# Kernel tuning notes

Hardware: AMD Instinct MI355X
Metric: run time of the kernel (lower is better)

Reference implementation:

```python
import jax, jax.numpy as jnp
import numpy as np

# LSS grid config (nuScenes defaults)
XB, YB, ZB = (-50.0, 50.0, 0.5), (-50.0, 50.0, 0.5), (-10.0, 10.0, 20.0)
DB = (4.0, 45.0, 1.0)
OGFH, OGFW, DOWNSAMPLE = 128, 352, 16
FH, FW = OGFH // DOWNSAMPLE, OGFW // DOWNSAMPLE  # 8, 22
DX = jnp.array([XB[2], YB[2], ZB[2]], jnp.float32)
BX = jnp.array([XB[0] + XB[2] / 2, YB[0] + YB[2] / 2, ZB[0] + ZB[2] / 2], jnp.float32)
NX = np.array([int((XB[1]-XB[0])/XB[2]), int((YB[1]-YB[0])/YB[2]), int((ZB[1]-ZB[0])/ZB[2])])  # [200,200,1]


def make_frustum():
    ds = jnp.arange(DB[0], DB[1], DB[2], dtype=jnp.float32)  # [D]
    D = ds.shape[0]
    xs = jnp.linspace(0.0, OGFW - 1.0, FW, dtype=jnp.float32)
    ys = jnp.linspace(0.0, OGFH - 1.0, FH, dtype=jnp.float32)
    xs_g = jnp.broadcast_to(xs[None, None, :], (D, FH, FW))
    ys_g = jnp.broadcast_to(ys[None, :, None], (D, FH, FW))
    ds_g = jnp.broadcast_to(ds[:, None, None], (D, FH, FW))
    return jnp.stack([xs_g, ys_g, ds_g], -1)  # [D,FH,FW,3]


def setup_inputs() -> dict:
    key = jax.random.key(0)
    ks = jax.random.split(key, 8)
    B, N, D, C = 8, 6, 41, 64
    x = jax.random.normal(ks[0], (B, N, D, FH, FW, C), jnp.float32)
    eye = jnp.eye(3, dtype=jnp.float32)
    rots = eye[None, None] + 0.01 * jax.random.normal(ks[1], (B, N, 3, 3), jnp.float32)
    trans = 0.5 * jax.random.normal(ks[2], (B, N, 3), jnp.float32)
    # realistic post-augmentation intrinsics for 352x128 images
    base_intrin = jnp.array([[250.0, 0.0, 176.0], [0.0, 250.0, 64.0], [0.0, 0.0, 1.0]], jnp.float32)
    intrins = base_intrin[None, None] + 0.1 * jax.random.normal(ks[3], (B, N, 3, 3), jnp.float32)
    post_rots = eye[None, None] + 0.001 * jax.random.normal(ks[4], (B, N, 3, 3), jnp.float32)
    post_trans = 0.1 * jax.random.normal(ks[5], (B, N, 3), jnp.float32)
    return {"x": x, "rots": rots, "trans": trans, "intrins": intrins,
            "post_rots": post_rots, "post_trans": post_trans}


def _get_geometry(frustum, rots, trans, intrins, post_rots, post_trans):
    eps = 1e-6
    eye = jnp.eye(3, dtype=post_rots.dtype)
    # undo post-augmentation
    pts = frustum[None, None] - post_trans[:, :, None, None, None, :]  # [B,N,D,H,W,3]
    inv_post = jnp.linalg.inv(post_rots + eye * eps)
    pts = jnp.einsum('bnij,bndhwj->bndhwi', inv_post, pts)
    xy, d = pts[..., :2], pts[..., 2:3]
    safe_d = jnp.where(jnp.abs(d) < eps, eps * jnp.sign(d + eps), d)
    pts = jnp.concatenate([xy * safe_d, safe_d], -1)
    combine = rots @ jnp.linalg.inv(intrins + eye * eps)  # [B,N,3,3]
    pts = jnp.einsum('bnij,bndhwj->bndhwi', combine, pts)
    return pts + trans[:, :, None, None, None, :]


def _voxel_pooling(geom, x):
    # geom: [B,N,D,H,W,3], x: [B,N,D,H,W,C]
    B, N, D, H, W, C = x.shape
    nx0, nx1, nx2 = int(NX[0]), int(NX[1]), int(NX[2])
    Nprime = B * N * D * H * W
    gn = (geom - (BX - DX / 2.0)) / DX
    gi = gn.astype(jnp.int32).reshape(Nprime, 3)  # trunc toward zero like .long()
    xf = x.reshape(Nprime, C)
    kept = ((gi[:, 0] >= 0) & (gi[:, 0] < nx0) &
            (gi[:, 1] >= 0) & (gi[:, 1] < nx1) &
            (gi[:, 2] >= 0) & (gi[:, 2] < nx2))
    xf = xf * kept[:, None].astype(xf.dtype)
    gx = jnp.clip(gi[:, 0], 0, nx0 - 1)
    gy = jnp.clip(gi[:, 1], 0, nx1 - 1)
    gz = jnp.clip(gi[:, 2], 0, nx2 - 1)
    batch_ix = jnp.repeat(jnp.arange(B, dtype=jnp.int32), Nprime // B)
    # sum-per-voxel (equivalent to sort + cumsum_trick + scatter-set)
    flat = ((batch_ix * nx2 + gz) * nx0 + gx) * nx1 + gy
    pooled = jax.ops.segment_sum(xf, flat, num_segments=B * nx2 * nx0 * nx1)
    final = pooled.reshape(B, nx2, nx0, nx1, C).transpose(0, 4, 1, 2, 3)
    return final  # [B,C,nz,nx,ny]


def reference(x, rots, trans, intrins, post_rots, post_trans):
    frustum = make_frustum()
    geom = _get_geometry(frustum, rots, trans, intrins, post_rots, post_trans)
    return _voxel_pooling(geom, x)
```

## Files before the change

### kernel.cpp

```cpp
#include <hip/hip_runtime.h>
#include <math.h>

namespace {

constexpr int B  = 8;
constexpr int N  = 6;
constexpr int D  = 41;
constexpr int FH = 8;
constexpr int FW = 22;
constexpr int C  = 64;
constexpr int NPTS = B * N * D * FH * FW;
constexpr int NX0 = 200, NX1 = 200, NX2 = 1;
constexpr int NVOX = NX0 * NX1;
constexpr int NVOX_ALL = B * NVOX;
constexpr int MAT_STRIDE = 24;
constexpr size_t SCR_ELEMS = (size_t)B * NVOX * C;
constexpr size_t SCR_BYTES = SCR_ELEMS * sizeof(float);
constexpr int VTILES = NVOX / 64;

__device__ inline void inv3x3(const float a[9], float r[9]) {
  float c00 = a[4] * a[8] - a[5] * a[7];
  float c01 = a[5] * a[6] - a[3] * a[8];
  float c02 = a[3] * a[7] - a[4] * a[6];
  float det = a[0] * c00 + a[1] * c01 + a[2] * c02;
  float id  = 1.0f / det;
  r[0] = c00 * id;
  r[1] = (a[2] * a[7] - a[1] * a[8]) * id;
  r[2] = (a[1] * a[5] - a[2] * a[4]) * id;
  r[3] = c01 * id;
  r[4] = (a[0] * a[8] - a[2] * a[6]) * id;
  r[5] = (a[2] * a[3] - a[0] * a[5]) * id;
  r[6] = c02 * id;
  r[7] = (a[1] * a[6] - a[0] * a[7]) * id;
  r[8] = (a[0] * a[4] - a[1] * a[3]) * id;
}

__device__ inline void build_mats(int i,
                                  const float* __restrict__ rots,
                                  const float* __restrict__ trans,
                                  const float* __restrict__ intrins,
                                  const float* __restrict__ post_rots,
                                  const float* __restrict__ post_trans,
                                  float* __restrict__ o) {
#pragma clang fp contract(off)
  const float eps = 1e-6f;
  float m[9], inv_post[9], ki[9];

  for (int k = 0; k < 9; ++k) m[k] = post_rots[i * 9 + k];
  m[0] += eps; m[4] += eps; m[8] += eps;
  inv3x3(m, inv_post);

  for (int k = 0; k < 9; ++k) m[k] = intrins[i * 9 + k];
  m[0] += eps; m[4] += eps; m[8] += eps;
  inv3x3(m, ki);

  for (int k = 0; k < 9; ++k) o[k] = inv_post[k];
  for (int r = 0; r < 3; ++r)
    for (int c = 0; c < 3; ++c)
      o[9 + r * 3 + c] = rots[i * 9 + r * 3 + 0] * ki[0 * 3 + c]
                       + rots[i * 9 + r * 3 + 1] * ki[1 * 3 + c]
                       + rots[i * 9 + r * 3 + 2] * ki[2 * 3 + c];
  for (int k = 0; k < 3; ++k) o[18 + k] = trans[i * 3 + k];
  for (int k = 0; k < 3; ++k) o[21 + k] = post_trans[i * 3 + k];
}

__device__ inline int point_voxel(int wid, const float* __restrict__ mats) {
#pragma clang fp contract(off)
  int t  = wid;
  int w  = t % FW;  t /= FW;
  int h  = t % FH;  t /= FH;
  int dd = t % D;   t /= D;
  int n  = t % N;
  int b  = t / N;

  const float* M = mats + (b * N + n) * MAT_STRIDE;

  float u   = (float)w * (351.0f / 21.0f);
  float v   = (float)h * (127.0f / 7.0f);
  float dep = 4.0f + (float)dd;

  float p0 = u - M[21], p1 = v - M[22], p2 = dep - M[23];

  float q0 = M[0] * p0 + M[1] * p1 + M[2] * p2;
  float q1 = M[3] * p0 + M[4] * p1 + M[5] * p2;
  float q2 = M[6] * p0 + M[7] * p1 + M[8] * p2;

  float sd;
  if (fabsf(q2) < 1e-6f) {
    float t2 = q2 + 1e-6f;
    float s  = (t2 > 0.0f) ? 1.0f : ((t2 < 0.0f) ? -1.0f : 0.0f);
    sd = 1e-6f * s;
  } else {
    sd = q2;
  }
  float r0 = q0 * sd, r1 = q1 * sd, r2 = sd;

  float g0 = (M[9]  * r0 + M[10] * r1 + M[11] * r2) + M[18];
  float g1 = (M[12] * r0 + M[13] * r1 + M[14] * r2) + M[19];
  float g2 = (M[15] * r0 + M[16] * r1 + M[17] * r2) + M[20];

  float gnx = (g0 + 50.0f) / 0.5f;
  float gny = (g1 + 50.0f) / 0.5f;
  float gnz = (g2 + 10.0f) / 20.0f;
  int gx = (int)gnx;
  int gy = (int)gny;
  int gz = (int)gnz;

  if (gx < 0 || gx >= NX0 || gy < 0 || gy >= NX1 || gz < 0 || gz >= NX2)
    return -1;
  return b * NVOX + gx * NX1 + gy;
}

__global__ __launch_bounds__(256) void mark_kernel(const float* __restrict__ rots,
                                                   const float* __restrict__ trans,
                                                   const float* __restrict__ intrins,
                                                   const float* __restrict__ post_rots,
                                                   const float* __restrict__ post_trans,
                                                   int* __restrict__ vox,
                                                   unsigned char* __restrict__ mask) {
  __shared__ float smats[B * N * MAT_STRIDE];
  int t = threadIdx.x;
  if (t < B * N)
    build_mats(t, rots, trans, intrins, post_rots, post_trans, smats + t * MAT_STRIDE);
  __syncthreads();

  int tid = blockIdx.x * 256 + t;
  int v = point_voxel(tid, smats);
  vox[tid] = v;
  if (v >= 0) mask[v] = 1;
}

__global__ __launch_bounds__(256) void zero_touched(const unsigned char* __restrict__ mask,
                                                    float* __restrict__ scratch) {
  int tid  = blockIdx.x * 256 + threadIdx.x;
  int lane = threadIdx.x & 63;
  int base = tid & ~63;

  bool touched = mask[tid] != 0;
  unsigned long long m = __ballot(touched);
  while (m) {
    int src = __ffsll((long long)m) - 1;
    m &= m - 1;
    int v = base + src;
    scratch[(size_t)v * C + lane] = 0.0f;
  }
}

__global__ __launch_bounds__(256) void splat_kernel(const float* __restrict__ x,
                                                    const int* __restrict__ vox,
                                                    float* __restrict__ scratch) {
  int tid  = blockIdx.x * 256 + threadIdx.x;
  int lane = threadIdx.x & 63;
  int base = tid & ~63;

  int v = vox[tid];
  unsigned long long m = __ballot(v >= 0);
  while (m) {
    int src = __ffsll((long long)m) - 1;
    m &= m - 1;
    int p  = base + src;
    int vv = __shfl(v, src);
    float val = x[(size_t)p * C + lane];
    atomicAdd(scratch + (size_t)vv * C + lane, val);
  }
}

__global__ __launch_bounds__(256) void transpose_out(const float* __restrict__ scratch,
                                                     const unsigned char* __restrict__ mask,
                                                     float* __restrict__ out) {
  __shared__ float lds[64][65];
  __shared__ int any_touched;
  int bt   = blockIdx.x;
  int b    = bt / VTILES;
  int tile = bt % VTILES;
  int v0   = tile * 64;
  int t    = threadIdx.x;

  const unsigned char* mrow = mask + (size_t)b * NVOX + v0;

  if (t == 0) any_touched = 0;
  __syncthreads();
  if (t < 64 && mrow[t]) any_touched = 1;
  __syncthreads();

  int vx4 = (t & 15) * 4;
  int cr  = t >> 4;

  if (!any_touched) {
    float4 z = make_float4(0.f, 0.f, 0.f, 0.f);
    for (int k = 0; k < 4; ++k) {
      int c = cr + k * 16;
      *(float4*)(out + ((size_t)(b * C + c)) * NVOX + v0 + vx4) = z;
    }
    return;
  }

  int c4 = (t & 15) * 4;
  int r  = t >> 4;
  for (int k = 0; k < 4; ++k) {
    int row = r + k * 16;
    float4 vv = make_float4(0.f, 0.f, 0.f, 0.f);
    if (mrow[row])
      vv = *(const float4*)(scratch + ((size_t)(b * NVOX + v0 + row)) * C + c4);
    lds[row][c4 + 0] = vv.x;
    lds[row][c4 + 1] = vv.y;
    lds[row][c4 + 2] = vv.z;
    lds[row][c4 + 3] = vv.w;
  }
  __syncthreads();

  for (int k = 0; k < 4; ++k) {
    int c = cr + k * 16;
    float4 vv;
    vv.x = lds[vx4 + 0][c];
    vv.y = lds[vx4 + 1][c];
    vv.z = lds[vx4 + 2][c];
    vv.w = lds[vx4 + 3][c];
    *(float4*)(out + ((size_t)(b * C + c)) * NVOX + v0 + vx4) = vv;
  }
}

__global__ void prep_mats(const float* __restrict__ rots,
                          const float* __restrict__ trans,
                          const float* __restrict__ intrins,
                          const float* __restrict__ post_rots,
                          const float* __restrict__ post_trans,
                          float* __restrict__ mats) {
  int i = blockIdx.x * blockDim.x + threadIdx.x;
  if (i >= B * N) return;
  build_mats(i, rots, trans, intrins, post_rots, post_trans, mats + i * MAT_STRIDE);
}

__global__ __launch_bounds__(256) void lss_splat_direct(const float* __restrict__ x,
                                                        const float* __restrict__ mats,
                                                        float* __restrict__ out) {
  int wid  = blockIdx.x * 4 + (threadIdx.x >> 6);
  if (wid >= NPTS) return;
  int lane = threadIdx.x & 63;
  int voxel = point_voxel(wid, mats);
  if (voxel < 0) return;
  int b = voxel / NVOX;
  int v = voxel % NVOX;
  float val = x[(size_t)wid * C + lane];
  size_t oidx = ((size_t)(b * C + lane)) * NVOX + v;
  atomicAdd(out + oidx, val);
}

}

extern "C" void kernel_launch(void* const* d_in, const int* in_sizes, int n_in,
                              void* d_out, int out_size, void* d_ws, size_t ws_size,
                              hipStream_t stream) {
  const float* x          = (const float*)d_in[0];
  const float* rots       = (const float*)d_in[1];
  const float* trans      = (const float*)d_in[2];
  const float* intrins    = (const float*)d_in[3];
  const float* post_rots  = (const float*)d_in[4];
  const float* post_trans = (const float*)d_in[5];
  float* out = (float*)d_out;

  const size_t mask_off = (SCR_BYTES + 255) & ~(size_t)255;
  const size_t vox_off  = (mask_off + (size_t)NVOX_ALL + 255) & ~(size_t)255;
  const size_t need     = vox_off + (size_t)NPTS * sizeof(int);

  if (ws_size >= need) {
    float*         scratch = (float*)d_ws;
    unsigned char* mask    = (unsigned char*)d_ws + mask_off;
    int*           vox     = (int*)((char*)d_ws + vox_off);

    hipMemsetAsync(mask, 0, (size_t)NVOX_ALL, stream);
    mark_kernel<<<NPTS / 256, 256, 0, stream>>>(rots, trans, intrins, post_rots,
                                                post_trans, vox, mask);
    zero_touched<<<NVOX_ALL / 256, 256, 0, stream>>>(mask, scratch);
    splat_kernel<<<NPTS / 256, 256, 0, stream>>>(x, vox, scratch);
    transpose_out<<<B * VTILES, 256, 0, stream>>>(scratch, mask, out);
  } else {
    float* mats = (float*)d_ws;
    hipMemsetAsync(d_out, 0, (size_t)out_size * sizeof(float), stream);
    prep_mats<<<1, 64, 0, stream>>>(rots, trans, intrins, post_rots, post_trans, mats);
    lss_splat_direct<<<(NPTS + 3) / 4, 256, 0, stream>>>(x, mats, out);
  }
}
```

Before: 57.30 us.

## Fuse scratch zeroing into mark kernel and pre-reduce duplicate voxels before atomics

Merges the mark pass with the scratch-zeroing pass, so touched voxel rows are zeroed directly from each wavefront's point list. Consecutive points falling in the same voxel are skipped during zeroing and summed in registers before a single atomicAdd. The memset is replaced by a vectorized clear kernel, and transpose_out uses a wave vote instead of shared-memory flags and barriers. This removes one launch, cuts redundant stores and atomic traffic, and trades them for a data-dependent inner loop with extra shuffles.

Measured after the change: 58.29 us. No clear change (+1.7%).

```diff
diff --git a/kernel.cpp b/kernel.cpp
--- a/kernel.cpp
+++ b/kernel.cpp
@@ -111,38 +111,42 @@
   return b * NVOX + gx * NX1 + gy;
 }
 
-__global__ __launch_bounds__(256) void mark_kernel(const float* __restrict__ rots,
-                                                   const float* __restrict__ trans,
-                                                   const float* __restrict__ intrins,
-                                                   const float* __restrict__ post_rots,
-                                                   const float* __restrict__ post_trans,
-                                                   int* __restrict__ vox,
-                                                   unsigned char* __restrict__ mask) {
+__global__ __launch_bounds__(256) void clear_mask(int4* __restrict__ mask4) {
+  const int n4 = NVOX_ALL / 16;
+  int i = blockIdx.x * 256 + threadIdx.x;
+  if (i < n4) mask4[i] = make_int4(0, 0, 0, 0);
+}
+
+__global__ __launch_bounds__(256) void mark_zero(const float* __restrict__ rots,
+                                                 const float* __restrict__ trans,
+                                                 const float* __restrict__ intrins,
+                                                 const float* __restrict__ post_rots,
+                                                 const float* __restrict__ post_trans,
+                                                 int* __restrict__ vox,
+                                                 unsigned char* __restrict__ mask,
+                                                 float* __restrict__ scratch) {
   __shared__ float smats[B * N * MAT_STRIDE];
   int t = threadIdx.x;
   if (t < B * N)
     build_mats(t, rots, trans, intrins, post_rots, post_trans, smats + t * MAT_STRIDE);
   __syncthreads();
 
-  int tid = blockIdx.x * 256 + t;
+  int tid  = blockIdx.x * 256 + t;
+  int lane = t & 63;
+
   int v = point_voxel(tid, smats);
   vox[tid] = v;
   if (v >= 0) mask[v] = 1;
-}
-
-__global__ __launch_bounds__(256) void zero_touched(const unsigned char* __restrict__ mask,
-                                                    float* __restrict__ scratch) {
-  int tid  = blockIdx.x * 256 + threadIdx.x;
-  int lane = threadIdx.x & 63;
-  int base = tid & ~63;
-
-  bool touched = mask[tid] != 0;
-  unsigned long long m = __ballot(touched);
+
+  unsigned long long m = __ballot(v >= 0);
+  int prev = -1;
   while (m) {
     int src = __ffsll((long long)m) - 1;
     m &= m - 1;
-    int v = base + src;
-    scratch[(size_t)v * C + lane] = 0.0f;
+    int vv = __shfl(v, src);
+    if (vv == prev) continue;
+    prev = vv;
+    scratch[(size_t)vv * C + lane] = 0.0f;
   }
 }
 
@@ -158,10 +162,16 @@
   while (m) {
     int src = __ffsll((long long)m) - 1;
     m &= m - 1;
-    int p  = base + src;
     int vv = __shfl(v, src);
-    float val = x[(size_t)p * C + lane];
-    atomicAdd(scratch + (size_t)vv * C + lane, val);
+    float acc = x[(size_t)(base + src) * C + lane];
+    while (m) {
+      int s2 = __ffsll((long long)m) - 1;
+      int v2 = __shfl(v, s2);
+      if (v2 != vv) break;
+      acc += x[(size_t)(base + s2) * C + lane];
+      m &= m - 1;
+    }
+    atomicAdd(scratch + (size_t)vv * C + lane, acc);
   }
 }
 
@@ -169,29 +179,24 @@
                                                      const unsigned char* __restrict__ mask,
                                                      float* __restrict__ out) {
   __shared__ float lds[64][65];
-  __shared__ int any_touched;
   int bt   = blockIdx.x;
   int b    = bt / VTILES;
-  int tile = bt % VTILES;
-  int v0   = tile * 64;
+  int tl   = bt % VTILES;
+  int v0   = tl * 64;
   int t    = threadIdx.x;
+  int lane = t & 63;
 
   const unsigned char* mrow = mask + (size_t)b * NVOX + v0;
 
-  if (t == 0) any_touched = 0;
-  __syncthreads();
-  if (t < 64 && mrow[t]) any_touched = 1;
-  __syncthreads();
+  bool touched = __any(mrow[lane] != 0);
 
   int vx4 = (t & 15) * 4;
   int cr  = t >> 4;
 
-  if (!any_touched) {
+  if (!touched) {
     float4 z = make_float4(0.f, 0.f, 0.f, 0.f);
-    for (int k = 0; k < 4; ++k) {
-      int c = cr + k * 16;
-      *(float4*)(out + ((size_t)(b * C + c)) * NVOX + v0 + vx4) = z;
-    }
+    for (int k = 0; k < 4; ++k)
+      *(float4*)(out + ((size_t)(b * C + cr + k * 16)) * NVOX + v0 + vx4) = z;
     return;
   }
 
@@ -268,10 +273,9 @@
     unsigned char* mask    = (unsigned char*)d_ws + mask_off;
     int*           vox     = (int*)((char*)d_ws + vox_off);
 
-    hipMemsetAsync(mask, 0, (size_t)NVOX_ALL, stream);
-    mark_kernel<<<NPTS / 256, 256, 0, stream>>>(rots, trans, intrins, post_rots,
-                                                post_trans, vox, mask);
-    zero_touched<<<NVOX_ALL / 256, 256, 0, stream>>>(mask, scratch);
+    clear_mask<<<(NVOX_ALL / 16 + 255) / 256, 256, 0, stream>>>((int4*)mask);
+    mark_zero<<<NPTS / 256, 256, 0, stream>>>(rots, trans, intrins, post_rots,
+                                              post_trans, vox, mask, scratch);
     splat_kernel<<<NPTS / 256, 256, 0, stream>>>(x, vox, scratch);
     transpose_out<<<B * VTILES, 256, 0, stream>>>(scratch, mask, out);
   } else {
```
